# Kernel tuning notes

Measured on AMD Instinct MI355X. Metric: run time of the kernel, lower is better.

## Reference

```python
import jax, jax.numpy as jnp
import numpy as np

N_NODES = 100000
N_EDGES = 1600000
IN_F = 256
OUT_F = 128


def setup_inputs() -> dict:
    key = jax.random.key(0)
    k1, k2, k3, k4, k5, k6 = jax.random.split(key, 6)
    x = jax.random.normal(k1, (N_NODES, IN_F), dtype=jnp.float32)
    edge_src = jax.random.randint(k2, (N_EDGES,), 0, N_NODES, dtype=jnp.int64)
    edge_dst = jax.random.randint(k3, (N_EDGES,), 0, N_NODES, dtype=jnp.int64)
    edge_weight = jax.random.uniform(k4, (N_EDGES,), dtype=jnp.float32)
    stdv = 1.0 / np.sqrt(OUT_F)
    w = jax.random.uniform(k5, (IN_F, OUT_F), dtype=jnp.float32, minval=-stdv, maxval=stdv)
    b = jax.random.uniform(k6, (OUT_F,), dtype=jnp.float32, minval=-stdv, maxval=stdv)
    return {"x": x, "edge_src": edge_src, "edge_dst": edge_dst,
            "edge_weight": edge_weight, "w": w, "b": b}


def reference(x, edge_src, edge_dst, edge_weight, w, b):
    # dense feature transform: [N, in] @ [in, out] -> [N, out]
    h = x @ w
    # sparse adjacency SpMM: out[i] = sum_{e: dst[e]==i} a[e] * h[src[e]]
    msgs = h[edge_src] * edge_weight[:, None]          # [E, out]
    agg = jax.ops.segment_sum(msgs, edge_dst, num_segments=N_NODES)
    return agg + b
```

## Files before the change

### kernel.cpp

```cpp
#include <hip/hip_runtime.h>

#define N_NODES 100000
#define N_EDGES 1600000
#define IN_F 256
#define OUT_F 128

#define NBUCK 1563
#define NCH   250
#define CH    6400
#define BCAP  2048

typedef __attribute__((ext_vector_type(8))) short bf16x8;
typedef __attribute__((ext_vector_type(4))) float f32x4;

static __device__ __forceinline__ unsigned f2bf_u(float f) {
    unsigned u = __float_as_uint(f);
    return (u + 0x7FFFu + ((u >> 16) & 1u)) >> 16;
}
static __device__ __forceinline__ float bf2f(short s) {
    return __uint_as_float(((unsigned)(unsigned short)s) << 16);
}
static __device__ __forceinline__ bf16x8 pack_bf16x8(float4 a, float4 b) {
    union { unsigned u[4]; bf16x8 v; } r;
    r.u[0] = f2bf_u(a.x) | (f2bf_u(a.y) << 16);
    r.u[1] = f2bf_u(a.z) | (f2bf_u(a.w) << 16);
    r.u[2] = f2bf_u(b.x) | (f2bf_u(b.y) << 16);
    r.u[3] = f2bf_u(b.z) | (f2bf_u(b.w) << 16);
    return r.v;
}

__global__ __launch_bounds__(1024) void init_kernel(int* __restrict__ gadd,
                                                    const float* __restrict__ w,
                                                    unsigned short* __restrict__ wtf) {
    const int t = threadIdx.x;
    if (blockIdx.x == 0) {
        for (int i = t; i < NBUCK; i += 1024) gadd[i] = 0;
        return;
    }
    const int id = (blockIdx.x - 1) * 1024 + t;
    const int f = id >> 6, lane = id & 63;
    const int ks = f >> 3, nt = f & 7;
    const int m = lane & 15, q = lane >> 4;
    const int row = nt * 16 + m;
    const int col0 = ks * 32 + q * 8;
    unsigned short* o = wtf + (size_t)f * 512 + lane * 8;
    #pragma unroll
    for (int j = 0; j < 8; ++j)
        o[j] = (unsigned short)f2bf_u(w[(size_t)(col0 + j) * OUT_F + row]);
}

__global__ __launch_bounds__(1024) void part_kernel(const int* __restrict__ edge_src,
                                                    const int* __restrict__ edge_dst,
                                                    const float* __restrict__ edge_weight,
                                                    int* __restrict__ gadd,
                                                    int2* __restrict__ part) {
    __shared__ int h[NBUCK];
    const int t = threadIdx.x;
    const int c = blockIdx.x;
    for (int i = t; i < NBUCK; i += 1024) h[i] = 0;
    __syncthreads();

    const int e0 = c * CH;
    const int4*   d4 = (const int4*)(edge_dst + e0);
    const int4*   s4 = (const int4*)(edge_src + e0);
    const float4* w4 = (const float4*)(edge_weight + e0);

    int4   dd[2];
    int4   ss[2];
    float4 ww[2];
    bool   val[2];
    #pragma unroll
    for (int i = 0; i < 2; ++i) {
        const int k = t + i * 1024;
        val[i] = (k < CH / 4);
        if (val[i]) {
            dd[i] = d4[k];
            ss[i] = s4[k];
            ww[i] = w4[k];
            atomicAdd(&h[dd[i].x >> 6], 1);
            atomicAdd(&h[dd[i].y >> 6], 1);
            atomicAdd(&h[dd[i].z >> 6], 1);
            atomicAdd(&h[dd[i].w >> 6], 1);
        }
    }
    __syncthreads();

    for (int i = t; i < NBUCK; i += 1024) {
        const int cnt = h[i];
        int base = 0;
        if (cnt > 0) base = atomicAdd(&gadd[i], cnt);
        h[i] = i * BCAP + base;
    }
    __syncthreads();

    #pragma unroll
    for (int i = 0; i < 2; ++i) {
        if (val[i]) {
            int b, pos;
            b = dd[i].x >> 6; pos = atomicAdd(&h[b], 1);
            if (pos < (b + 1) * BCAP)
                part[pos] = make_int2(ss[i].x | ((dd[i].x & 63) << 24), __float_as_int(ww[i].x));
            b = dd[i].y >> 6; pos = atomicAdd(&h[b], 1);
            if (pos < (b + 1) * BCAP)
                part[pos] = make_int2(ss[i].y | ((dd[i].y & 63) << 24), __float_as_int(ww[i].y));
            b = dd[i].z >> 6; pos = atomicAdd(&h[b], 1);
            if (pos < (b + 1) * BCAP)
                part[pos] = make_int2(ss[i].z | ((dd[i].z & 63) << 24), __float_as_int(ww[i].z));
            b = dd[i].w >> 6; pos = atomicAdd(&h[b], 1);
            if (pos < (b + 1) * BCAP)
                part[pos] = make_int2(ss[i].w | ((dd[i].w & 63) << 24), __float_as_int(ww[i].w));
        }
    }
}

__global__ __launch_bounds__(256) void gemm_mfma_kernel(const float* __restrict__ x,
                                                        const unsigned short* __restrict__ wtf,
                                                        unsigned short* __restrict__ hb) {
    const int t = threadIdx.x;
    const int wave = t >> 6, lane = t & 63;
    const int m = lane & 15, quad = lane >> 4;
    const int row0 = blockIdx.x * 128 + wave * 32;

    int rA = row0 + m;      if (rA >= N_NODES) rA = N_NODES - 1;
    int rB = row0 + 16 + m; if (rB >= N_NODES) rB = N_NODES - 1;
    const float4* xA = (const float4*)(x + (size_t)rA * IN_F) + quad * 2;
    const float4* xB = (const float4*)(x + (size_t)rB * IN_F) + quad * 2;

    f32x4 acc[2][8];
    #pragma unroll
    for (int tl = 0; tl < 2; ++tl)
        #pragma unroll
        for (int nt = 0; nt < 8; ++nt) acc[tl][nt] = (f32x4){0.f, 0.f, 0.f, 0.f};

    const bf16x8* wf = (const bf16x8*)wtf;
    #pragma unroll
    for (int ks = 0; ks < 8; ++ks) {
        const bf16x8 a0 = pack_bf16x8(xA[ks * 8], xA[ks * 8 + 1]);
        const bf16x8 a1 = pack_bf16x8(xB[ks * 8], xB[ks * 8 + 1]);
        #pragma unroll
        for (int nt = 0; nt < 8; ++nt) {
            const bf16x8 bf = wf[(size_t)(ks * 8 + nt) * 64 + lane];
            acc[0][nt] = __builtin_amdgcn_mfma_f32_16x16x32_bf16(a0, bf, acc[0][nt], 0, 0, 0);
            acc[1][nt] = __builtin_amdgcn_mfma_f32_16x16x32_bf16(a1, bf, acc[1][nt], 0, 0, 0);
        }
    }

    #pragma unroll
    for (int tl = 0; tl < 2; ++tl) {
        const int tile_base = row0 + tl * 16;
        #pragma unroll
        for (int nt = 0; nt < 8; ++nt) {
            #pragma unroll
            for (int r = 0; r < 4; ++r) {
                const int orow = tile_base + quad * 4 + r;
                if (orow < N_NODES)
                    hb[(size_t)orow * OUT_F + nt * 16 + m] = (unsigned short)f2bf_u(acc[tl][nt][r]);
            }
        }
    }
}

__global__ __launch_bounds__(512) void spmm_kernel(const unsigned short* __restrict__ hb,
                                                   const int* __restrict__ gadd,
                                                   const int2* __restrict__ part,
                                                   const float* __restrict__ b,
                                                   float* __restrict__ out) {
    __shared__ int lh[64];
    __shared__ int lstart[65];
    __shared__ int lcur[64];
    __shared__ int2 list[BCAP];

    const int t = threadIdx.x;
    const int bucket = blockIdx.x;
    const int base = bucket * 64;

    int cntb = gadd[bucket];
    if (cntb > BCAP) cntb = BCAP;
    const size_t s0 = (size_t)bucket * BCAP;

    if (t < 64) lh[t] = 0;
    __syncthreads();

    int2 stash[4];
    int  sn[4];
    #pragma unroll
    for (int sub = 0; sub < 4; ++sub) {
        const int idx = sub * 512 + t;
        sn[sub] = -1;
        if (idx < cntb) {
            const int2 en = part[s0 + idx];
            const int n = ((unsigned)en.x) >> 24;
            sn[sub] = n;
            stash[sub] = make_int2(en.x & 0xFFFFFF, en.y);
            atomicAdd(&lh[n], 1);
        }
    }
    __syncthreads();

    if (t < 64) {
        const int v = lh[t];
        int s = v;
        #pragma unroll
        for (int off = 1; off < 64; off <<= 1) {
            const int o = __shfl_up(s, off);
            if (t >= off) s += o;
        }
        lstart[t] = s - v;
        lcur[t]   = s - v;
        if (t == 63) lstart[64] = s;
    }
    __syncthreads();

    #pragma unroll
    for (int sub = 0; sub < 4; ++sub) {
        if (sn[sub] >= 0) {
            const int pos = atomicAdd(&lcur[sn[sub]], 1);
            list[pos] = stash[sub];
        }
    }
    __syncthreads();

    const int j = t & 15;
    const float4* b4 = (const float4*)b;
    const float4 bb0 = b4[j * 2];
    const float4 bb1 = b4[j * 2 + 1];

    #pragma unroll
    for (int g = 0; g < 2; ++g) {
        const int n = g * 32 + (t >> 4);
        const int node = base + n;
        if (node >= N_NODES) continue;
        float4 acc0 = bb0, acc1 = bb1;
        int p = lstart[n];
        const int p1 = lstart[n + 1];
        for (; p + 4 <= p1; p += 4) {
            const int2 sw0 = list[p];
            const int2 sw1 = list[p + 1];
            const int2 sw2 = list[p + 2];
            const int2 sw3 = list[p + 3];
            const bf16x8 h0 = *(const bf16x8*)(hb + (size_t)sw0.x * OUT_F + j * 8);
            const bf16x8 h1 = *(const bf16x8*)(hb + (size_t)sw1.x * OUT_F + j * 8);
            const bf16x8 h2 = *(const bf16x8*)(hb + (size_t)sw2.x * OUT_F + j * 8);
            const bf16x8 h3 = *(const bf16x8*)(hb + (size_t)sw3.x * OUT_F + j * 8);
            const float w0 = __int_as_float(sw0.y);
            const float w1 = __int_as_float(sw1.y);
            const float w2 = __int_as_float(sw2.y);
            const float w3 = __int_as_float(sw3.y);
            acc0.x += w0 * bf2f(h0[0]); acc0.y += w0 * bf2f(h0[1]);
            acc0.z += w0 * bf2f(h0[2]); acc0.w += w0 * bf2f(h0[3]);
            acc1.x += w0 * bf2f(h0[4]); acc1.y += w0 * bf2f(h0[5]);
            acc1.z += w0 * bf2f(h0[6]); acc1.w += w0 * bf2f(h0[7]);
            acc0.x += w1 * bf2f(h1[0]); acc0.y += w1 * bf2f(h1[1]);
            acc0.z += w1 * bf2f(h1[2]); acc0.w += w1 * bf2f(h1[3]);
            acc1.x += w1 * bf2f(h1[4]); acc1.y += w1 * bf2f(h1[5]);
            acc1.z += w1 * bf2f(h1[6]); acc1.w += w1 * bf2f(h1[7]);
            acc0.x += w2 * bf2f(h2[0]); acc0.y += w2 * bf2f(h2[1]);
            acc0.z += w2 * bf2f(h2[2]); acc0.w += w2 * bf2f(h2[3]);
            acc1.x += w2 * bf2f(h2[4]); acc1.y += w2 * bf2f(h2[5]);
            acc1.z += w2 * bf2f(h2[6]); acc1.w += w2 * bf2f(h2[7]);
            acc0.x += w3 * bf2f(h3[0]); acc0.y += w3 * bf2f(h3[1]);
            acc0.z += w3 * bf2f(h3[2]); acc0.w += w3 * bf2f(h3[3]);
            acc1.x += w3 * bf2f(h3[4]); acc1.y += w3 * bf2f(h3[5]);
            acc1.z += w3 * bf2f(h3[6]); acc1.w += w3 * bf2f(h3[7]);
        }
        for (; p < p1; ++p) {
            const int2 sw = list[p];
            const float wgt = __int_as_float(sw.y);
            const bf16x8 hv = *(const bf16x8*)(hb + (size_t)sw.x * OUT_F + j * 8);
            acc0.x += wgt * bf2f(hv[0]); acc0.y += wgt * bf2f(hv[1]);
            acc0.z += wgt * bf2f(hv[2]); acc0.w += wgt * bf2f(hv[3]);
            acc1.x += wgt * bf2f(hv[4]); acc1.y += wgt * bf2f(hv[5]);
            acc1.z += wgt * bf2f(hv[6]); acc1.w += wgt * bf2f(hv[7]);
        }
        float4* o4 = (float4*)(out + (size_t)node * OUT_F + j * 8);
        o4[0] = acc0;
        o4[1] = acc1;
    }
}

extern "C" void kernel_launch(void* const* d_in, const int* in_sizes, int n_in,
                              void* d_out, int out_size, void* d_ws, size_t ws_size,
                              hipStream_t stream) {
    const float* x           = (const float*)d_in[0];
    const int*   edge_src    = (const int*)d_in[1];
    const int*   edge_dst    = (const int*)d_in[2];
    const float* edge_weight = (const float*)d_in[3];
    const float* w           = (const float*)d_in[4];
    const float* b           = (const float*)d_in[5];
    float* out = (float*)d_out;

    char* ws = (char*)d_ws;
    size_t off = 0;
    unsigned short* hb  = (unsigned short*)(ws + off);
    off += (size_t)N_NODES * OUT_F * 2;           off = (off + 15) & ~(size_t)15;
    unsigned short* wtf = (unsigned short*)(ws + off);
    off += (size_t)IN_F * OUT_F * 2;              off = (off + 15) & ~(size_t)15;
    int* gadd = (int*)(ws + off);
    off += (size_t)NBUCK * 4;                     off = (off + 15) & ~(size_t)15;
    int2* part = (int2*)(ws + off);
    off += (size_t)NBUCK * BCAP * 8;

    init_kernel<<<5, 1024, 0, stream>>>(gadd, w, wtf);
    part_kernel<<<NCH, 1024, 0, stream>>>(edge_src, edge_dst, edge_weight, gadd, part);
    gemm_mfma_kernel<<<(N_NODES + 127) / 128, 256, 0, stream>>>(x, wtf, hb);
    spmm_kernel<<<NBUCK, 512, 0, stream>>>(hb, gadd, part, b, out);
}
```

Baseline: 285.4 us.

## Stripe bucket counters across eight sub-regions and split SpMM launch in two

The partition kernel now hands out bucket slots through eight striped counters, one per chunk stripe, and each stripe writes into its own 256-entry sub-region of the bucket. The aim is to reduce global atomic contention on the shared per-bucket counters. The SpMM kernel gathers the eight sub-regions using a prefix sum of their counts. SpMM is also split into two launches over halves of the buckets. Each stripe is capped at 256 edges, so a skewed distribution could drop edges that the old 2048 cap would have kept. The extra launch adds overhead.

```diff
diff --git a/kernel.cpp b/kernel.cpp
--- a/kernel.cpp
+++ b/kernel.cpp
@@ -9,6 +9,8 @@
 #define NCH   250
 #define CH    6400
 #define BCAP  2048
+#define SCAP  256
+#define HALF  782
 
 typedef __attribute__((ext_vector_type(8))) short bf16x8;
 typedef __attribute__((ext_vector_type(4))) float f32x4;
@@ -34,7 +36,7 @@
                                                     unsigned short* __restrict__ wtf) {
     const int t = threadIdx.x;
     if (blockIdx.x == 0) {
-        for (int i = t; i < NBUCK; i += 1024) gadd[i] = 0;
+        for (int i = t; i < 8 * NBUCK; i += 1024) gadd[i] = 0;
         return;
     }
     const int id = (blockIdx.x - 1) * 1024 + t;
@@ -57,6 +59,8 @@
     __shared__ int h[NBUCK];
     const int t = threadIdx.x;
     const int c = blockIdx.x;
+    const int stripe = c & 7;
+    const int sbase = stripe << 8;
     for (int i = t; i < NBUCK; i += 1024) h[i] = 0;
     __syncthreads();
 
@@ -85,11 +89,12 @@
     }
     __syncthreads();
 
+    int* g = gadd + stripe * NBUCK;
     for (int i = t; i < NBUCK; i += 1024) {
         const int cnt = h[i];
         int base = 0;
-        if (cnt > 0) base = atomicAdd(&gadd[i], cnt);
-        h[i] = i * BCAP + base;
+        if (cnt > 0) base = atomicAdd(&g[i], cnt);
+        h[i] = (i << 11) + sbase + base;
     }
     __syncthreads();
 
@@ -98,16 +103,16 @@
         if (val[i]) {
             int b, pos;
             b = dd[i].x >> 6; pos = atomicAdd(&h[b], 1);
-            if (pos < (b + 1) * BCAP)
+            if (pos < (b << 11) + sbase + SCAP)
                 part[pos] = make_int2(ss[i].x | ((dd[i].x & 63) << 24), __float_as_int(ww[i].x));
             b = dd[i].y >> 6; pos = atomicAdd(&h[b], 1);
-            if (pos < (b + 1) * BCAP)
+            if (pos < (b << 11) + sbase + SCAP)
                 part[pos] = make_int2(ss[i].y | ((dd[i].y & 63) << 24), __float_as_int(ww[i].y));
             b = dd[i].z >> 6; pos = atomicAdd(&h[b], 1);
-            if (pos < (b + 1) * BCAP)
+            if (pos < (b << 11) + sbase + SCAP)
                 part[pos] = make_int2(ss[i].z | ((dd[i].z & 63) << 24), __float_as_int(ww[i].z));
             b = dd[i].w >> 6; pos = atomicAdd(&h[b], 1);
-            if (pos < (b + 1) * BCAP)
+            if (pos < (b << 11) + sbase + SCAP)
                 part[pos] = make_int2(ss[i].w | ((dd[i].w & 63) << 24), __float_as_int(ww[i].w));
         }
     }
@@ -160,26 +165,36 @@
     }
 }
 
-__global__ __launch_bounds__(512) void spmm_kernel(const unsigned short* __restrict__ hb,
-                                                   const int* __restrict__ gadd,
-                                                   const int2* __restrict__ part,
-                                                   const float* __restrict__ b,
-                                                   float* __restrict__ out) {
+static __device__ __forceinline__ void spmm_body(const int bucket,
+                                                 const unsigned short* __restrict__ hb,
+                                                 const int* __restrict__ gadd,
+                                                 const int2* __restrict__ part,
+                                                 const float* __restrict__ b,
+                                                 float* __restrict__ out) {
     __shared__ int lh[64];
     __shared__ int lstart[65];
     __shared__ int lcur[64];
+    __shared__ int cs[8];
+    __shared__ int csum[9];
     __shared__ int2 list[BCAP];
 
     const int t = threadIdx.x;
-    const int bucket = blockIdx.x;
     const int base = bucket * 64;
 
-    int cntb = gadd[bucket];
-    if (cntb > BCAP) cntb = BCAP;
-    const size_t s0 = (size_t)bucket * BCAP;
-
     if (t < 64) lh[t] = 0;
-    __syncthreads();
+    if (t < 8) {
+        int cc = gadd[t * NBUCK + bucket];
+        cs[t] = cc > SCAP ? SCAP : cc;
+    }
+    __syncthreads();
+    if (t == 0) {
+        int a = 0;
+        csum[0] = 0;
+        #pragma unroll
+        for (int i = 0; i < 8; ++i) { a += cs[i]; csum[i + 1] = a; }
+    }
+    __syncthreads();
+    const int total = csum[8];
 
     int2 stash[4];
     int  sn[4];
@@ -187,8 +202,12 @@
     for (int sub = 0; sub < 4; ++sub) {
         const int idx = sub * 512 + t;
         sn[sub] = -1;
-        if (idx < cntb) {
-            const int2 en = part[s0 + idx];
+        if (idx < total) {
+            int sdx = 0;
+            #pragma unroll
+            for (int q = 1; q < 8; ++q) sdx += (idx >= csum[q]);
+            const int local = idx - csum[sdx];
+            const int2 en = part[((size_t)bucket << 11) + (sdx << 8) + local];
             const int n = ((unsigned)en.x) >> 24;
             sn[sub] = n;
             stash[sub] = make_int2(en.x & 0xFFFFFF, en.y);
@@ -278,6 +297,21 @@
     }
 }
 
+__global__ __launch_bounds__(512) void spmm_a_kernel(const unsigned short* __restrict__ hb,
+                                                     const int* __restrict__ gadd,
+                                                     const int2* __restrict__ part,
+                                                     const float* __restrict__ b,
+                                                     float* __restrict__ out) {
+    spmm_body(blockIdx.x, hb, gadd, part, b, out);
+}
+__global__ __launch_bounds__(512) void spmm_b_kernel(const unsigned short* __restrict__ hb,
+                                                     const int* __restrict__ gadd,
+                                                     const int2* __restrict__ part,
+                                                     const float* __restrict__ b,
+                                                     float* __restrict__ out) {
+    spmm_body(blockIdx.x + HALF, hb, gadd, part, b, out);
+}
+
 extern "C" void kernel_launch(void* const* d_in, const int* in_sizes, int n_in,
                               void* d_out, int out_size, void* d_ws, size_t ws_size,
                               hipStream_t stream) {
@@ -296,12 +330,13 @@
     unsigned short* wtf = (unsigned short*)(ws + off);
     off += (size_t)IN_F * OUT_F * 2;              off = (off + 15) & ~(size_t)15;
     int* gadd = (int*)(ws + off);
-    off += (size_t)NBUCK * 4;                     off = (off + 15) & ~(size_t)15;
+    off += (size_t)8 * NBUCK * 4;                 off = (off + 15) & ~(size_t)15;
     int2* part = (int2*)(ws + off);
     off += (size_t)NBUCK * BCAP * 8;
 
     init_kernel<<<5, 1024, 0, stream>>>(gadd, w, wtf);
     part_kernel<<<NCH, 1024, 0, stream>>>(edge_src, edge_dst, edge_weight, gadd, part);
     gemm_mfma_kernel<<<(N_NODES + 127) / 128, 256, 0, stream>>>(x, wtf, hb);
-    spmm_kernel<<<NBUCK, 512, 0, stream>>>(hb, gadd, part, b, out);
-}
+    spmm_a_kernel<<<HALF, 512, 0, stream>>>(hb, gadd, part, b, out);
+    spmm_b_kernel<<<NBUCK - HALF, 512, 0, stream>>>(hb, gadd, part, b, out);
+}
```

After: 288.8 us. About the same (+1.2%).
